# Kernel optimization log

Measured on AMD Instinct MI355X. Metric: run time of the kernel, lower is better.

The kernel has to match this reference:

```python
import jax, jax.numpy as jnp
import numpy as np

N1, N2 = 262144, 65536          # dense / coarse point counts (packed batch)
PREV, SKIP, M0, M1 = 512, 256, 256, 256
EPS_BN = 1e-5                    # torch BatchNorm1d default eps
EPS_DIST = 1e-8


def _bn(x, g, b):
    # BatchNorm1d in training mode: biased batch stats over the point axis
    m = x.mean(axis=0)
    v = x.var(axis=0)
    return (x - m) * jax.lax.rsqrt(v + EPS_BN) * g + b


def setup_inputs() -> dict:
    key = jax.random.key(0)
    ks = jax.random.split(key, 8)
    inp = {
        "points1": jax.random.normal(ks[0], (N1, SKIP), jnp.float32),
        "points2": jax.random.normal(ks[1], (N2, PREV), jnp.float32),
        "dist": jax.random.uniform(ks[2], (N1, 3), jnp.float32),
        "idx": jax.random.randint(ks[3], (N1, 3), 0, N2, dtype=jnp.int32),
        # mlp_f0 / norm_f0
        "Wf0": jax.random.normal(ks[4], (PREV, M0), jnp.float32) / np.sqrt(PREV).astype(np.float32),
        "bf0": jnp.zeros((M0,), jnp.float32),
        "gf0": jnp.ones((M0,), jnp.float32),
        "betaf0": jnp.zeros((M0,), jnp.float32),
        # mlp_s0 / norm_s0 (skip path)
        "Ws0": jax.random.normal(ks[5], (SKIP, M0), jnp.float32) / np.sqrt(SKIP).astype(np.float32),
        "bs0": jnp.zeros((M0,), jnp.float32),
        "gs0": jnp.ones((M0,), jnp.float32),
        "betas0": jnp.zeros((M0,), jnp.float32),
        # mlp_convs[0] / mlp_bns[0]
        "W1": jax.random.normal(ks[6], (M0, M1), jnp.float32) / np.sqrt(M0).astype(np.float32),
        "b1": jnp.zeros((M1,), jnp.float32),
        "g1": jnp.ones((M1,), jnp.float32),
        "beta1": jnp.zeros((M1,), jnp.float32),
    }
    return inp


def reference(points1, points2, dist, idx, Wf0, bf0, gf0, betaf0,
              Ws0, bs0, gs0, betas0, W1, b1, g1, beta1):
    # f0 MLP + BN on coarse features: [N2, PREV] -> [N2, M0]
    p2 = _bn(points2 @ Wf0 + bf0, gf0, betaf0)
    # inverse-distance weights over 3 neighbors: [N1, 3]
    dr = 1.0 / (dist + EPS_DIST)
    w = dr / dr.sum(axis=1, keepdims=True)
    # fused gather + weighted sum: p2[idx] is [N1, 3, M0]
    interp = jnp.einsum('nkc,nk->nc', p2[idx], w)
    # skip path: [N1, SKIP] -> [N1, M0]
    skip = _bn(points1 @ Ws0 + bs0, gs0, betas0)
    x = jax.nn.relu(interp + skip)
    # mlp_convs stack (one layer here): Linear + BN + ReLU
    x = jax.nn.relu(_bn(x @ W1 + b1, g1, beta1))
    return x
```

## Files before the change

kernel.cpp:

```cpp
#include <hip/hip_runtime.h>
#include <hip/hip_bf16.h>

#define CN1 262144
#define CN2 65536
#define CPREV 512
#define CSKIP 256

using u16 = unsigned short;

typedef __attribute__((ext_vector_type(8))) short short8;
typedef __attribute__((ext_vector_type(8))) unsigned short ushort8;
typedef __attribute__((ext_vector_type(4))) float f32x4;
typedef __attribute__((ext_vector_type(8))) float f32x8;

__device__ __forceinline__ float toF(float v) { return v; }
__device__ __forceinline__ float toF(u16 u) { return __uint_as_float(((unsigned)u) << 16); }
__device__ __forceinline__ u16 f2bf(float f) {
    unsigned b = __float_as_uint(f);
    b += 0x7FFFu + ((b >> 16) & 1u);
    return (u16)(b >> 16);
}
__device__ __forceinline__ unsigned pack2(float lo, float hi) {
    return ((unsigned)f2bf(hi) << 16) | (unsigned)f2bf(lo);
}

__global__ __launch_bounds__(256) void transpose_all(
    const float* __restrict__ Wf0, const float* __restrict__ Ws0,
    const float* __restrict__ W1,
    u16* __restrict__ Wtf0, u16* __restrict__ Wts0, u16* __restrict__ Wt1)
{
    int b = blockIdx.x;
    const float* W; u16* Wt; int ksh, e;
    if (b < 512)      { W = Wf0; Wt = Wtf0; ksh = 9; e = b * 256 + threadIdx.x; }
    else if (b < 768) { W = Ws0; Wt = Wts0; ksh = 8; e = (b - 512) * 256 + threadIdx.x; }
    else              { W = W1;  Wt = Wt1;  ksh = 8; e = (b - 768) * 256 + threadIdx.x; }
    int K = 1 << ksh;
    int n = e >> ksh;
    int k = e & (K - 1);
    Wt[e] = f2bf(W[((size_t)k << 8) + n]);
}

template<typename OT>
__device__ __forceinline__ void epilogue(
    f32x4 (&acc)[4][4], u16* AsU, u16* BsU,
    const float* __restrict__ bias, OT* __restrict__ C,
    float* __restrict__ partial, int bm, int t)
{
    const int lane = t & 63;
    const int wid = t >> 6;
    const int wrow = wid >> 2;
    const int wcol = wid & 3;
    __syncthreads();
    float* cs  = (float*)AsU;
    float* cs2 = ((float*)AsU) + 512;
    const int r4 = (lane >> 4) * 4;
    const int cc = lane & 15;
    float bv[4];
#pragma unroll
    for (int ni = 0; ni < 4; ++ni) bv[ni] = bias[wcol * 64 + ni * 16 + cc];

#pragma unroll
    for (int ni = 0; ni < 4; ++ni) {
        int col = wcol * 64 + ni * 16 + cc;
        float s = 0.f, s2 = 0.f;
#pragma unroll
        for (int mi = 0; mi < 4; ++mi) {
#pragma unroll
            for (int j = 0; j < 4; ++j) {
                float val = acc[mi][ni][j] + bv[ni];
                s += val;
                s2 = fmaf(val, val, s2);
            }
        }
        s  += __shfl_xor(s, 16);  s  += __shfl_xor(s, 32);
        s2 += __shfl_xor(s2, 16); s2 += __shfl_xor(s2, 32);
        if (lane < 16) { cs[wrow * 256 + col] = s; cs2[wrow * 256 + col] = s2; }
    }

    if constexpr (sizeof(OT) == 2) {
        u16* patchw = BsU + wid * (16 * 72);
        const int trow = lane >> 2;
        const int c16 = (lane & 3) * 16;
#pragma unroll
        for (int mi = 0; mi < 4; ++mi) {
            __syncthreads();
#pragma unroll
            for (int ni = 0; ni < 4; ++ni)
#pragma unroll
                for (int j = 0; j < 4; ++j)
                    patchw[(r4 + j) * 72 + ni * 16 + cc] = f2bf(acc[mi][ni][j] + bv[ni]);
            __syncthreads();
            ushort8 u0 = *(const ushort8*)&patchw[trow * 72 + c16];
            ushort8 u1 = *(const ushort8*)&patchw[trow * 72 + c16 + 8];
            size_t r = (size_t)bm + wrow * 64 + mi * 16 + trow;
            size_t cb = (size_t)wcol * 64 + c16;
            *(ushort8*)((u16*)C + r * 256 + cb) = u0;
            *(ushort8*)((u16*)C + r * 256 + cb + 8) = u1;
        }
    } else {
        float* patchf = ((float*)BsU) + wid * (16 * 36);
        const int trow = lane >> 2;
        const int c8 = (lane & 3) * 8;
#pragma unroll
        for (int mi = 0; mi < 4; ++mi) {
#pragma unroll
            for (int np = 0; np < 2; ++np) {
                __syncthreads();
#pragma unroll
                for (int h = 0; h < 2; ++h) {
                    int ni = np * 2 + h;
#pragma unroll
                    for (int j = 0; j < 4; ++j)
                        patchf[(r4 + j) * 36 + h * 16 + cc] = acc[mi][ni][j] + bv[ni];
                }
                __syncthreads();
                float4 v0 = *(float4*)&patchf[trow * 36 + c8];
                float4 v1 = *(float4*)&patchf[trow * 36 + c8 + 4];
                size_t r = (size_t)bm + wrow * 64 + mi * 16 + trow;
                size_t cb = (size_t)wcol * 64 + np * 32 + c8;
                *(float4*)((float*)C + r * 256 + cb) = v0;
                *(float4*)((float*)C + r * 256 + cb + 4) = v1;
            }
        }
    }
    __syncthreads();
    if (t < 256) {
        partial[(size_t)blockIdx.x * 512 + t]       = cs[t] + cs[256 + t];
        partial[(size_t)blockIdx.x * 512 + 256 + t] = cs2[t] + cs2[256 + t];
    }
}

template<int K, typename OT>
__global__ __launch_bounds__(512) void gemm_mfma(
    const float* __restrict__ Af, const u16* __restrict__ Wt,
    const float* __restrict__ bias, OT* __restrict__ C,
    float* __restrict__ partial)
{
    __shared__ u16 As0[128 * 40], As1[128 * 40];
    __shared__ u16 Bs0[256 * 40], Bs1[256 * 40];
    const int t = threadIdx.x;
    const int bm = blockIdx.x * 128;
    const int lane = t & 63;
    const int wid = t >> 6;
    const int wrow = wid >> 2;
    const int wcol = wid & 3;

    const int arow = t >> 2;
    const int koff = (t & 3) * 8;

    f32x4 acc[4][4] = {};

    float4 ga0A, ga1A, ga0B, ga1B;
    ushort8 gb0A, gb1A, gb0B, gb1B;

    auto LOADA = [&](int k0) {
        const float* p = Af + (size_t)(bm + arow) * K + k0 + koff;
        ga0A = *(const float4*)p;
        ga1A = *(const float4*)(p + 4);
        const u16* q = Wt + (size_t)arow * K + k0 + koff;
        gb0A = *(const ushort8*)q;
        gb1A = *(const ushort8*)(q + (size_t)128 * K);
    };
    auto LOADB = [&](int k0) {
        const float* p = Af + (size_t)(bm + arow) * K + k0 + koff;
        ga0B = *(const float4*)p;
        ga1B = *(const float4*)(p + 4);
        const u16* q = Wt + (size_t)arow * K + k0 + koff;
        gb0B = *(const ushort8*)q;
        gb1B = *(const ushort8*)(q + (size_t)128 * K);
    };
    auto STAGE = [&](u16* as, u16* bs, const float4& g0, const float4& g1,
                     const ushort8& b0, const ushort8& b1) {
        uint4 w;
        w.x = pack2(g0.x, g0.y);
        w.y = pack2(g0.z, g0.w);
        w.z = pack2(g1.x, g1.y);
        w.w = pack2(g1.z, g1.w);
        *(uint4*)&as[arow * 40 + koff] = w;
        *(ushort8*)&bs[arow * 40 + koff] = b0;
        *(ushort8*)&bs[(128 + arow) * 40 + koff] = b1;
    };
    auto MMA = [&](const u16* as, const u16* bs) {
        const int kq = (lane >> 4) * 8;
        const int rr = lane & 15;
        short8 af[4];
#pragma unroll
        for (int mi = 0; mi < 4; ++mi)
            af[mi] = *(const short8*)&as[(wrow * 64 + mi * 16 + rr) * 40 + kq];
#pragma unroll
        for (int ni = 0; ni < 4; ++ni) {
            short8 bf = *(const short8*)&bs[(wcol * 64 + ni * 16 + rr) * 40 + kq];
#pragma unroll
            for (int mi = 0; mi < 4; ++mi)
                acc[mi][ni] = __builtin_amdgcn_mfma_f32_16x16x32_bf16(
                    af[mi], bf, acc[mi][ni], 0, 0, 0);
        }
    };

    constexpr int nk = K >> 5;
    LOADA(0);
    LOADB(32);
    STAGE(As0, Bs0, ga0A, ga1A, gb0A, gb1A);
    __syncthreads();

#define GM_STEP(IT)                                                           \
    if ((IT) < nk) {                                                          \
        if ((IT) + 2 < nk) {                                                  \
            if (((IT)&1) == 0) LOADA(((IT)+2) << 5); else LOADB(((IT)+2) << 5);\
        }                                                                     \
        if ((IT) + 1 < nk) {                                                  \
            if (((IT)&1) == 0) STAGE(As1, Bs1, ga0B, ga1B, gb0B, gb1B);       \
            else               STAGE(As0, Bs0, ga0A, ga1A, gb0A, gb1A);       \
        }                                                                     \
        MMA((((IT)&1) == 0) ? As0 : As1, (((IT)&1) == 0) ? Bs0 : Bs1);        \
        __syncthreads();                                                      \
    }
    GM_STEP(0)  GM_STEP(1)  GM_STEP(2)  GM_STEP(3)
    GM_STEP(4)  GM_STEP(5)  GM_STEP(6)  GM_STEP(7)
    GM_STEP(8)  GM_STEP(9)  GM_STEP(10) GM_STEP(11)
    GM_STEP(12) GM_STEP(13) GM_STEP(14) GM_STEP(15)
#undef GM_STEP

    epilogue<OT>(acc, As0, Bs0, bias, C, partial, bm, t);
}

template<typename OT>
__global__ __launch_bounds__(512) void gemm_fused(
    const u16* __restrict__ skipb, const u16* __restrict__ y2,
    const float* __restrict__ dist, const int* __restrict__ idx,
    const float* __restrict__ ssf, const float* __restrict__ sss,
    const u16* __restrict__ Wt, const float* __restrict__ bias,
    OT* __restrict__ C, float* __restrict__ partial)
{
    constexpr int K = 256;
    __shared__ u16 As0[128 * 40], As1[128 * 40];
    __shared__ u16 Bs0[256 * 40], Bs1[256 * 40];
    __shared__ float sstab[768];
    const int t = threadIdx.x;
    const int bm = blockIdx.x * 128;
    const int lane = t & 63;
    const int wid = t >> 6;
    const int wrow = wid >> 2;
    const int wcol = wid & 3;

    const int arow = t >> 2;
    const int koff = (t & 3) * 8;
    const int row = bm + arow;

    for (int e = t; e < 768; e += 512)
        sstab[e] = (e < 256) ? ssf[e] : sss[e - 256];

    float d0 = dist[row * 3 + 0], d1 = dist[row * 3 + 1], d2 = dist[row * 3 + 2];
    float r0 = 1.f / (d0 + 1e-8f), r1 = 1.f / (d1 + 1e-8f), r2 = 1.f / (d2 + 1e-8f);
    float inv = 1.f / (r0 + r1 + r2);
    const float w0 = r0 * inv, w1 = r1 * inv, w2 = r2 * inv;
    const size_t i0 = (size_t)idx[row * 3 + 0];
    const size_t i1 = (size_t)idx[row * 3 + 1];
    const size_t i2 = (size_t)idx[row * 3 + 2];

    f32x4 acc[4][4] = {};

    ushort8 skA, a0A, a1A, a2A, gb0A, gb1A;
    ushort8 skB, a0B, a1B, a2B, gb0B, gb1B;

    auto LOADA = [&](int k0) {
        const int kc = k0 + koff;
        skA = *(const ushort8*)(skipb + (size_t)row * 256 + kc);
        a0A = *(const ushort8*)(y2 + i0 * 256 + kc);
        a1A = *(const ushort8*)(y2 + i1 * 256 + kc);
        a2A = *(const ushort8*)(y2 + i2 * 256 + kc);
        const u16* q = Wt + (size_t)arow * K + kc;
        gb0A = *(const ushort8*)q;
        gb1A = *(const ushort8*)(q + (size_t)128 * K);
    };
    auto LOADB = [&](int k0) {
        const int kc = k0 + koff;
        skB = *(const ushort8*)(skipb + (size_t)row * 256 + kc);
        a0B = *(const ushort8*)(y2 + i0 * 256 + kc);
        a1B = *(const ushort8*)(y2 + i1 * 256 + kc);
        a2B = *(const ushort8*)(y2 + i2 * 256 + kc);
        const u16* q = Wt + (size_t)arow * K + kc;
        gb0B = *(const ushort8*)q;
        gb1B = *(const ushort8*)(q + (size_t)128 * K);
    };
    auto STAGE = [&](u16* as, u16* bs, int kstep, const ushort8& sk8,
                     const ushort8& a0, const ushort8& a1, const ushort8& a2,
                     const ushort8& b0, const ushort8& b1) {
        const int kc = (kstep << 5) + koff;
        f32x8 sf = *(const f32x8*)&sstab[kc];
        f32x8 sx = *(const f32x8*)&sstab[256 + kc];
        f32x8 ch = *(const f32x8*)&sstab[512 + kc];
        float xs[8];
#pragma unroll
        for (int j = 0; j < 8; ++j) {
            float iv = w0 * toF((u16)a0[j]) + w1 * toF((u16)a1[j])
                     + w2 * toF((u16)a2[j]);
            float val = fmaf(iv, sf[j], fmaf(toF((u16)sk8[j]), sx[j], ch[j]));
            xs[j] = fmaxf(val, 0.f);
        }
        uint4 w;
        w.x = pack2(xs[0], xs[1]);
        w.y = pack2(xs[2], xs[3]);
        w.z = pack2(xs[4], xs[5]);
        w.w = pack2(xs[6], xs[7]);
        *(uint4*)&as[arow * 40 + koff] = w;
        *(ushort8*)&bs[arow * 40 + koff] = b0;
        *(ushort8*)&bs[(128 + arow) * 40 + koff] = b1;
    };
    auto MMA = [&](const u16* as, const u16* bs) {
        const int kq = (lane >> 4) * 8;
        const int rr = lane & 15;
        short8 af[4];
#pragma unroll
        for (int mi = 0; mi < 4; ++mi)
            af[mi] = *(const short8*)&as[(wrow * 64 + mi * 16 + rr) * 40 + kq];
#pragma unroll
        for (int ni = 0; ni < 4; ++ni) {
            short8 bf = *(const short8*)&bs[(wcol * 64 + ni * 16 + rr) * 40 + kq];
#pragma unroll
            for (int mi = 0; mi < 4; ++mi)
                acc[mi][ni] = __builtin_amdgcn_mfma_f32_16x16x32_bf16(
                    af[mi], bf, acc[mi][ni], 0, 0, 0);
        }
    };

    constexpr int nk = K >> 5;
    LOADA(0);
    LOADB(32);
    __syncthreads();
    STAGE(As0, Bs0, 0, skA, a0A, a1A, a2A, gb0A, gb1A);
    __syncthreads();

#define GF_STEP(IT)                                                           \
    if ((IT) < nk) {                                                          \
        if ((IT) + 2 < nk) {                                                  \
            if (((IT)&1) == 0) LOADA(((IT)+2) << 5); else LOADB(((IT)+2) << 5);\
        }                                                                     \
        if ((IT) + 1 < nk) {                                                  \
            if (((IT)&1) == 0)                                                \
                STAGE(As1, Bs1, (IT)+1, skB, a0B, a1B, a2B, gb0B, gb1B);      \
            else                                                              \
                STAGE(As0, Bs0, (IT)+1, skA, a0A, a1A, a2A, gb0A, gb1A);      \
        }                                                                     \
        MMA((((IT)&1) == 0) ? As0 : As1, (((IT)&1) == 0) ? Bs0 : Bs1);        \
        __syncthreads();                                                      \
    }
    GF_STEP(0) GF_STEP(1) GF_STEP(2) GF_STEP(3)
    GF_STEP(4) GF_STEP(5) GF_STEP(6) GF_STEP(7)
#undef GF_STEP

    epilogue<OT>(acc, As0, Bs0, bias, C, partial, bm, t);
}

__global__ __launch_bounds__(256) void colstats_final_par(
    const float* __restrict__ partial, int nb, float invR,
    const float* __restrict__ g, const float* __restrict__ beta,
    const float* __restrict__ fold, float* __restrict__ ss)
{
    int c = blockIdx.x;
    int t = threadIdx.x;
    float s = 0.f, s2 = 0.f;
    for (int b = t; b < nb; b += 256) {
        s  += partial[(size_t)b * 512 + c];
        s2 += partial[(size_t)b * 512 + 256 + c];
    }
#pragma unroll
    for (int o = 32; o > 0; o >>= 1) {
        s += __shfl_xor(s, o);
        s2 += __shfl_xor(s2, o);
    }
    __shared__ float rs[4], rs2[4];
    if ((t & 63) == 0) { rs[t >> 6] = s; rs2[t >> 6] = s2; }
    __syncthreads();
    if (t == 0) {
        float S  = rs[0] + rs[1] + rs[2] + rs[3];
        float S2 = rs2[0] + rs2[1] + rs2[2] + rs2[3];
        float m = S * invR;
        float var = fmaf(-m, m, S2 * invR);
        float scale = g[c] * rsqrtf(var + 1e-5f);
        float shift = fmaf(-m, scale, beta[c]);
        if (fold) shift += fold[256 + c];
        ss[c] = scale;
        ss[256 + c] = shift;
    }
}

__global__ __launch_bounds__(256) void bn_relu_cvt(
    const u16* __restrict__ y3, float* __restrict__ out,
    const float* __restrict__ ss)
{
    size_t e = ((size_t)blockIdx.x * 256 + threadIdx.x) * 8;
    int kc = (int)(e & 255);
    ushort8 v = *(const ushort8*)(y3 + e);
    f32x8 sc = *(const f32x8*)(ss + kc);
    f32x8 sh = *(const f32x8*)(ss + 256 + kc);
    float4 o0, o1;
    o0.x = fmaxf(fmaf(toF((u16)v[0]), sc[0], sh[0]), 0.f);
    o0.y = fmaxf(fmaf(toF((u16)v[1]), sc[1], sh[1]), 0.f);
    o0.z = fmaxf(fmaf(toF((u16)v[2]), sc[2], sh[2]), 0.f);
    o0.w = fmaxf(fmaf(toF((u16)v[3]), sc[3], sh[3]), 0.f);
    o1.x = fmaxf(fmaf(toF((u16)v[4]), sc[4], sh[4]), 0.f);
    o1.y = fmaxf(fmaf(toF((u16)v[5]), sc[5], sh[5]), 0.f);
    o1.z = fmaxf(fmaf(toF((u16)v[6]), sc[6], sh[6]), 0.f);
    o1.w = fmaxf(fmaf(toF((u16)v[7]), sc[7], sh[7]), 0.f);
    *(float4*)(out + e) = o0;
    *(float4*)(out + e + 4) = o1;
}

__global__ __launch_bounds__(256) void bn_relu_inplace(
    float* __restrict__ out, const float* __restrict__ ss)
{
    size_t i4 = (size_t)blockIdx.x * 256 + threadIdx.x;
    int c4 = (int)(i4 & 63);
    float4 v = reinterpret_cast<float4*>(out)[i4];
    float4 sc = reinterpret_cast<const float4*>(ss)[c4];
    float4 sh = reinterpret_cast<const float4*>(ss + 256)[c4];
    v.x = fmaxf(fmaf(v.x, sc.x, sh.x), 0.f);
    v.y = fmaxf(fmaf(v.y, sc.y, sh.y), 0.f);
    v.z = fmaxf(fmaf(v.z, sc.z, sh.z), 0.f);
    v.w = fmaxf(fmaf(v.w, sc.w, sh.w), 0.f);
    reinterpret_cast<float4*>(out)[i4] = v;
}

extern "C" void kernel_launch(void* const* d_in, const int* in_sizes, int n_in,
                              void* d_out, int out_size, void* d_ws, size_t ws_size,
                              hipStream_t stream) {
    const float* points1 = (const float*)d_in[0];
    const float* points2 = (const float*)d_in[1];
    const float* dist    = (const float*)d_in[2];
    const int*   idx     = (const int*)d_in[3];
    const float* Wf0     = (const float*)d_in[4];
    const float* bf0     = (const float*)d_in[5];
    const float* gf0     = (const float*)d_in[6];
    const float* betaf0  = (const float*)d_in[7];
    const float* Ws0     = (const float*)d_in[8];
    const float* bs0     = (const float*)d_in[9];
    const float* gs0     = (const float*)d_in[10];
    const float* betas0  = (const float*)d_in[11];
    const float* W1      = (const float*)d_in[12];
    const float* b1      = (const float*)d_in[13];
    const float* g1      = (const float*)d_in[14];
    const float* beta1   = (const float*)d_in[15];

    u16* ws = (u16*)d_ws;
    size_t off = 0;
    u16* y2   = ws + off;  off += (size_t)CN2 * 256;
    u16* xbuf = ws + off;  off += (size_t)CN1 * 256;
    u16* Wtf0 = ws + off;  off += 512 * 256;
    u16* Wts0 = ws + off;  off += 256 * 256;
    u16* Wt1  = ws + off;  off += 256 * 256;
    float* partial = (float*)(ws + off); off += (size_t)2048 * 512 * 2;
    float* ss_f0 = (float*)(ws + off); off += 1024;
    float* ss_s0 = (float*)(ws + off); off += 1024;
    float* ss_1  = (float*)(ws + off); off += 1024;
    u16* y3 = ws + off;
    const size_t NEED = (off + (size_t)CN1 * 256) * 2;
    const bool fused_y3 = (ws_size >= NEED);
    float* out = (float*)d_out;

    transpose_all<<<1024, 256, 0, stream>>>(Wf0, Ws0, W1, Wtf0, Wts0, Wt1);

    gemm_mfma<512, u16><<<CN2 / 128, 512, 0, stream>>>(
        points2, Wtf0, bf0, y2, partial);
    colstats_final_par<<<256, 256, 0, stream>>>(partial, CN2 / 128, 1.0f / CN2,
                                                gf0, betaf0, nullptr, ss_f0);
    gemm_mfma<256, u16><<<CN1 / 128, 512, 0, stream>>>(
        points1, Wts0, bs0, xbuf, partial);
    colstats_final_par<<<256, 256, 0, stream>>>(partial, CN1 / 128, 1.0f / CN1,
                                                gs0, betas0, ss_f0, ss_s0);
    if (fused_y3) {
        gemm_fused<u16><<<CN1 / 128, 512, 0, stream>>>(
            xbuf, y2, dist, idx, ss_f0, ss_s0, Wt1, b1, y3, partial);
    } else {
        gemm_fused<float><<<CN1 / 128, 512, 0, stream>>>(
            xbuf, y2, dist, idx, ss_f0, ss_s0, Wt1, b1, out, partial);
    }
    colstats_final_par<<<256, 256, 0, stream>>>(partial, CN1 / 128, 1.0f / CN1,
                                                g1, beta1, nullptr, ss_1);
    if (fused_y3) {
        bn_relu_cvt<<<32768, 256, 0, stream>>>(y3, out, ss_1);
    } else {
        bn_relu_inplace<<<CN1 / 4, 256, 0, stream>>>(out, ss_1);
    }
}
```

Baseline: 416.7 us.

## Load GEMM weight fragments directly from global into registers, drop B LDS staging

Both MFMA GEMM kernels no longer stage weight tiles through shared memory. Each wave now loads its bf16 B fragments straight from global memory into double-buffered registers, one k-step ahead. The epilogue reuses the A buffers for its patch scratch, and the BN partial-sum write moves ahead of the output stores. The kernels also get minimum-occupancy launch bounds. This cuts LDS traffic and footprint and removes B-tile LDS stores, but adds redundant global/L2 weight reads per wave. The occupancy bounds may force register spills given the 64-register accumulator.

```diff
diff --git a/kernel.cpp b/kernel.cpp
--- a/kernel.cpp
+++ b/kernel.cpp
@@ -42,7 +42,7 @@
 
 template<typename OT>
 __device__ __forceinline__ void epilogue(
-    f32x4 (&acc)[4][4], u16* AsU, u16* BsU,
+    f32x4 (&acc)[4][4], u16* As0, u16* As1,
     const float* __restrict__ bias, OT* __restrict__ C,
     float* __restrict__ partial, int bm, int t)
 {
@@ -51,8 +51,8 @@
     const int wrow = wid >> 2;
     const int wcol = wid & 3;
     __syncthreads();
-    float* cs  = (float*)AsU;
-    float* cs2 = ((float*)AsU) + 512;
+    float* cs  = (float*)As0;
+    float* cs2 = ((float*)As0) + 512;
     const int r4 = (lane >> 4) * 4;
     const int cc = lane & 15;
     float bv[4];
@@ -76,9 +76,14 @@
         s2 += __shfl_xor(s2, 16); s2 += __shfl_xor(s2, 32);
         if (lane < 16) { cs[wrow * 256 + col] = s; cs2[wrow * 256 + col] = s2; }
     }
+    __syncthreads();
+    if (t < 256) {
+        partial[(size_t)blockIdx.x * 512 + t]       = cs[t] + cs[256 + t];
+        partial[(size_t)blockIdx.x * 512 + 256 + t] = cs2[t] + cs2[256 + t];
+    }
 
     if constexpr (sizeof(OT) == 2) {
-        u16* patchw = BsU + wid * (16 * 72);
+        u16* patchw = (wid < 4) ? (As0 + wid * 1152) : (As1 + (wid - 4) * 1152);
         const int trow = lane >> 2;
         const int c16 = (lane & 3) * 16;
 #pragma unroll
@@ -98,7 +103,7 @@
             *(ushort8*)((u16*)C + r * 256 + cb + 8) = u1;
         }
     } else {
-        float* patchf = ((float*)BsU) + wid * (16 * 36);
+        float* patchf = (float*)((wid < 4) ? (As0 + wid * 1152) : (As1 + (wid - 4) * 1152));
         const int trow = lane >> 2;
         const int c8 = (lane & 3) * 8;
 #pragma unroll
@@ -123,21 +128,15 @@
             }
         }
     }
-    __syncthreads();
-    if (t < 256) {
-        partial[(size_t)blockIdx.x * 512 + t]       = cs[t] + cs[256 + t];
-        partial[(size_t)blockIdx.x * 512 + 256 + t] = cs2[t] + cs2[256 + t];
-    }
 }
 
 template<int K, typename OT>
-__global__ __launch_bounds__(512) void gemm_mfma(
+__global__ __launch_bounds__(512, 4) void gemm_mfma(
     const float* __restrict__ Af, const u16* __restrict__ Wt,
     const float* __restrict__ bias, OT* __restrict__ C,
     float* __restrict__ partial)
 {
     __shared__ u16 As0[128 * 40], As1[128 * 40];
-    __shared__ u16 Bs0[256 * 40], Bs1[256 * 40];
     const int t = threadIdx.x;
     const int bm = blockIdx.x * 128;
     const int lane = t & 63;
@@ -147,73 +146,69 @@
 
     const int arow = t >> 2;
     const int koff = (t & 3) * 8;
+    const int rr = lane & 15;
+    const int kq = (lane >> 4) * 8;
+    const u16* Wb = Wt + (size_t)(wcol * 64 + rr) * K + kq;
 
     f32x4 acc[4][4] = {};
 
     float4 ga0A, ga1A, ga0B, ga1B;
-    ushort8 gb0A, gb1A, gb0B, gb1B;
+    short8 bfA[4], bfB[4];
 
     auto LOADA = [&](int k0) {
         const float* p = Af + (size_t)(bm + arow) * K + k0 + koff;
         ga0A = *(const float4*)p;
         ga1A = *(const float4*)(p + 4);
-        const u16* q = Wt + (size_t)arow * K + k0 + koff;
-        gb0A = *(const ushort8*)q;
-        gb1A = *(const ushort8*)(q + (size_t)128 * K);
     };
     auto LOADB = [&](int k0) {
         const float* p = Af + (size_t)(bm + arow) * K + k0 + koff;
         ga0B = *(const float4*)p;
         ga1B = *(const float4*)(p + 4);
-        const u16* q = Wt + (size_t)arow * K + k0 + koff;
-        gb0B = *(const ushort8*)q;
-        gb1B = *(const ushort8*)(q + (size_t)128 * K);
-    };
-    auto STAGE = [&](u16* as, u16* bs, const float4& g0, const float4& g1,
-                     const ushort8& b0, const ushort8& b1) {
+    };
+    auto LOADBF = [&](int k0, short8 (&bf)[4]) {
+#pragma unroll
+        for (int ni = 0; ni < 4; ++ni)
+            bf[ni] = *(const short8*)(Wb + (size_t)ni * 16 * K + k0);
+    };
+    auto STAGE = [&](u16* as, const float4& g0, const float4& g1) {
         uint4 w;
         w.x = pack2(g0.x, g0.y);
         w.y = pack2(g0.z, g0.w);
         w.z = pack2(g1.x, g1.y);
         w.w = pack2(g1.z, g1.w);
         *(uint4*)&as[arow * 40 + koff] = w;
-        *(ushort8*)&bs[arow * 40 + koff] = b0;
-        *(ushort8*)&bs[(128 + arow) * 40 + koff] = b1;
-    };
-    auto MMA = [&](const u16* as, const u16* bs) {
-        const int kq = (lane >> 4) * 8;
-        const int rr = lane & 15;
+    };
+    auto MMA = [&](const u16* as, const short8 (&bf)[4]) {
         short8 af[4];
 #pragma unroll
         for (int mi = 0; mi < 4; ++mi)
             af[mi] = *(const short8*)&as[(wrow * 64 + mi * 16 + rr) * 40 + kq];
 #pragma unroll
-        for (int ni = 0; ni < 4; ++ni) {
-            short8 bf = *(const short8*)&bs[(wcol * 64 + ni * 16 + rr) * 40 + kq];
+        for (int ni = 0; ni < 4; ++ni)
 #pragma unroll
             for (int mi = 0; mi < 4; ++mi)
                 acc[mi][ni] = __builtin_amdgcn_mfma_f32_16x16x32_bf16(
-                    af[mi], bf, acc[mi][ni], 0, 0, 0);
-        }
+                    af[mi], bf[ni], acc[mi][ni], 0, 0, 0);
     };
 
     constexpr int nk = K >> 5;
     LOADA(0);
     LOADB(32);
-    STAGE(As0, Bs0, ga0A, ga1A, gb0A, gb1A);
-    __syncthreads();
-
-#define GM_STEP(IT)                                                           \
-    if ((IT) < nk) {                                                          \
-        if ((IT) + 2 < nk) {                                                  \
-            if (((IT)&1) == 0) LOADA(((IT)+2) << 5); else LOADB(((IT)+2) << 5);\
-        }                                                                     \
-        if ((IT) + 1 < nk) {                                                  \
-            if (((IT)&1) == 0) STAGE(As1, Bs1, ga0B, ga1B, gb0B, gb1B);       \
-            else               STAGE(As0, Bs0, ga0A, ga1A, gb0A, gb1A);       \
-        }                                                                     \
-        MMA((((IT)&1) == 0) ? As0 : As1, (((IT)&1) == 0) ? Bs0 : Bs1);        \
-        __syncthreads();                                                      \
+    STAGE(As0, ga0A, ga1A);
+    LOADBF(0, bfA);
+    __syncthreads();
+
+#define GM_STEP(IT)                                                             \
+    if ((IT) < nk) {                                                            \
+        if ((IT) + 2 < nk) {                                                    \
+            if (((IT)&1) == 0) LOADA(((IT)+2) << 5); else LOADB(((IT)+2) << 5); \
+        }                                                                       \
+        if ((IT) + 1 < nk) {                                                    \
+            if (((IT)&1) == 0) { STAGE(As1, ga0B, ga1B); LOADBF(((IT)+1) << 5, bfB); } \
+            else               { STAGE(As0, ga0A, ga1A); LOADBF(((IT)+1) << 5, bfA); } \
+        }                                                                       \
+        if (((IT)&1) == 0) MMA(As0, bfA); else MMA(As1, bfB);                   \
+        __syncthreads();                                                        \
     }
     GM_STEP(0)  GM_STEP(1)  GM_STEP(2)  GM_STEP(3)
     GM_STEP(4)  GM_STEP(5)  GM_STEP(6)  GM_STEP(7)
@@ -221,11 +216,11 @@
     GM_STEP(12) GM_STEP(13) GM_STEP(14) GM_STEP(15)
 #undef GM_STEP
 
-    epilogue<OT>(acc, As0, Bs0, bias, C, partial, bm, t);
+    epilogue<OT>(acc, As0, As1, bias, C, partial, bm, t);
 }
 
 template<typename OT>
-__global__ __launch_bounds__(512) void gemm_fused(
+__global__ __launch_bounds__(512, 3) void gemm_fused(
     const u16* __restrict__ skipb, const u16* __restrict__ y2,
     const float* __restrict__ dist, const int* __restrict__ idx,
     const float* __restrict__ ssf, const float* __restrict__ sss,
@@ -234,7 +229,6 @@
 {
     constexpr int K = 256;
     __shared__ u16 As0[128 * 40], As1[128 * 40];
-    __shared__ u16 Bs0[256 * 40], Bs1[256 * 40];
     __shared__ float sstab[768];
     const int t = threadIdx.x;
     const int bm = blockIdx.x * 128;
@@ -246,6 +240,9 @@
     const int arow = t >> 2;
     const int koff = (t & 3) * 8;
     const int row = bm + arow;
+    const int rr = lane & 15;
+    const int kq = (lane >> 4) * 8;
+    const u16* Wb = Wt + (size_t)(wcol * 64 + rr) * K + kq;
 
     for (int e = t; e < 768; e += 512)
         sstab[e] = (e < 256) ? ssf[e] : sss[e - 256];
@@ -254,38 +251,37 @@
     float r0 = 1.f / (d0 + 1e-8f), r1 = 1.f / (d1 + 1e-8f), r2 = 1.f / (d2 + 1e-8f);
     float inv = 1.f / (r0 + r1 + r2);
     const float w0 = r0 * inv, w1 = r1 * inv, w2 = r2 * inv;
-    const size_t i0 = (size_t)idx[row * 3 + 0];
-    const size_t i1 = (size_t)idx[row * 3 + 1];
-    const size_t i2 = (size_t)idx[row * 3 + 2];
+    const unsigned i0 = (unsigned)idx[row * 3 + 0];
+    const unsigned i1 = (unsigned)idx[row * 3 + 1];
+    const unsigned i2 = (unsigned)idx[row * 3 + 2];
 
     f32x4 acc[4][4] = {};
 
-    ushort8 skA, a0A, a1A, a2A, gb0A, gb1A;
-    ushort8 skB, a0B, a1B, a2B, gb0B, gb1B;
+    ushort8 skA, a0A, a1A, a2A;
+    ushort8 skB, a0B, a1B, a2B;
+    short8 bfA[4], bfB[4];
 
     auto LOADA = [&](int k0) {
         const int kc = k0 + koff;
         skA = *(const ushort8*)(skipb + (size_t)row * 256 + kc);
-        a0A = *(const ushort8*)(y2 + i0 * 256 + kc);
-        a1A = *(const ushort8*)(y2 + i1 * 256 + kc);
-        a2A = *(const ushort8*)(y2 + i2 * 256 + kc);
-        const u16* q = Wt + (size_t)arow * K + kc;
-        gb0A = *(const ushort8*)q;
-        gb1A = *(const ushort8*)(q + (size_t)128 * K);
+        a0A = *(const ushort8*)(y2 + (size_t)i0 * 256 + kc);
+        a1A = *(const ushort8*)(y2 + (size_t)i1 * 256 + kc);
+        a2A = *(const ushort8*)(y2 + (size_t)i2 * 256 + kc);
     };
     auto LOADB = [&](int k0) {
         const int kc = k0 + koff;
         skB = *(const ushort8*)(skipb + (size_t)row * 256 + kc);
-        a0B = *(const ushort8*)(y2 + i0 * 256 + kc);
-        a1B = *(const ushort8*)(y2 + i1 * 256 + kc);
-        a2B = *(const ushort8*)(y2 + i2 * 256 + kc);
-        const u16* q = Wt + (size_t)arow * K + kc;
-        gb0B = *(const ushort8*)q;
-        gb1B = *(const ushort8*)(q + (size_t)128 * K);
-    };
-    auto STAGE = [&](u16* as, u16* bs, int kstep, const ushort8& sk8,
-                     const ushort8& a0, const ushort8& a1, const ushort8& a2,
-                     const ushort8& b0, const ushort8& b1) {
+        a0B = *(const ushort8*)(y2 + (size_t)i0 * 256 + kc);
+        a1B = *(const ushort8*)(y2 + (size_t)i1 * 256 + kc);
+        a2B = *(const ushort8*)(y2 + (size_t)i2 * 256 + kc);
+    };
+    auto LOADBF = [&](int k0, short8 (&bf)[4]) {
+#pragma unroll
+        for (int ni = 0; ni < 4; ++ni)
+            bf[ni] = *(const short8*)(Wb + (size_t)ni * 16 * K + k0);
+    };
+    auto STAGE = [&](u16* as, int kstep, const ushort8& sk8,
+                     const ushort8& a0, const ushort8& a1, const ushort8& a2) {
         const int kc = (kstep << 5) + koff;
         f32x8 sf = *(const f32x8*)&sstab[kc];
         f32x8 sx = *(const f32x8*)&sstab[256 + kc];
@@ -304,52 +300,47 @@
         w.z = pack2(xs[4], xs[5]);
         w.w = pack2(xs[6], xs[7]);
         *(uint4*)&as[arow * 40 + koff] = w;
-        *(ushort8*)&bs[arow * 40 + koff] = b0;
-        *(ushort8*)&bs[(128 + arow) * 40 + koff] = b1;
-    };
-    auto MMA = [&](const u16* as, const u16* bs) {
-        const int kq = (lane >> 4) * 8;
-        const int rr = lane & 15;
+    };
+    auto MMA = [&](const u16* as, const short8 (&bf)[4]) {
         short8 af[4];
 #pragma unroll
         for (int mi = 0; mi < 4; ++mi)
             af[mi] = *(const short8*)&as[(wrow * 64 + mi * 16 + rr) * 40 + kq];
 #pragma unroll
-        for (int ni = 0; ni < 4; ++ni) {
-            short8 bf = *(const short8*)&bs[(wcol * 64 + ni * 16 + rr) * 40 + kq];
+        for (int ni = 0; ni < 4; ++ni)
 #pragma unroll
             for (int mi = 0; mi < 4; ++mi)
                 acc[mi][ni] = __builtin_amdgcn_mfma_f32_16x16x32_bf16(
-                    af[mi], bf, acc[mi][ni], 0, 0, 0);
-        }
+                    af[mi], bf[ni], acc[mi][ni], 0, 0, 0);
     };
 
     constexpr int nk = K >> 5;
     LOADA(0);
     LOADB(32);
     __syncthreads();
-    STAGE(As0, Bs0, 0, skA, a0A, a1A, a2A, gb0A, gb1A);
-    __syncthreads();
-
-#define GF_STEP(IT)                                                           \
-    if ((IT) < nk) {                                                          \
-        if ((IT) + 2 < nk) {                                                  \
-            if (((IT)&1) == 0) LOADA(((IT)+2) << 5); else LOADB(((IT)+2) << 5);\
-        }                                                                     \
-        if ((IT) + 1 < nk) {                                                  \
-            if (((IT)&1) == 0)                                                \
-                STAGE(As1, Bs1, (IT)+1, skB, a0B, a1B, a2B, gb0B, gb1B);      \
-            else                                                              \
-                STAGE(As0, Bs0, (IT)+1, skA, a0A, a1A, a2A, gb0A, gb1A);      \
-        }                                                                     \
-        MMA((((IT)&1) == 0) ? As0 : As1, (((IT)&1) == 0) ? Bs0 : Bs1);        \
-        __syncthreads();                                                      \
+    STAGE(As0, 0, skA, a0A, a1A, a2A);
+    LOADBF(0, bfA);
+    __syncthreads();
+
+#define GF_STEP(IT)                                                             \
+    if ((IT) < nk) {                                                            \
+        if ((IT) + 2 < nk) {                                                    \
+            if (((IT)&1) == 0) LOADA(((IT)+2) << 5); else LOADB(((IT)+2) << 5); \
+        }                                                                       \
+        if ((IT) + 1 < nk) {                                                    \
+            if (((IT)&1) == 0) { STAGE(As1, (IT)+1, skB, a0B, a1B, a2B);        \
+                                 LOADBF(((IT)+1) << 5, bfB); }                  \
+            else               { STAGE(As0, (IT)+1, skA, a0A, a1A, a2A);        \
+                                 LOADBF(((IT)+1) << 5, bfA); }                  \
+        }                                                                       \
+        if (((IT)&1) == 0) MMA(As0, bfA); else MMA(As1, bfB);                   \
+        __syncthreads();                                                        \
     }
     GF_STEP(0) GF_STEP(1) GF_STEP(2) GF_STEP(3)
     GF_STEP(4) GF_STEP(5) GF_STEP(6) GF_STEP(7)
 #undef GF_STEP
 
-    epilogue<OT>(acc, As0, Bs0, bias, C, partial, bm, t);
+    epilogue<OT>(acc, As0, As1, bias, C, partial, bm, t);
 }
 
 __global__ __launch_bounds__(256) void colstats_final_par(
```

Result: slower. 479.3 us (+15.0%).

## Double GEMM block size to 16 waves with split A/B loader roles

Applied to the files above, without the earlier changes.

The three MFMA GEMM kernels now launch 1024 threads per block instead of 512, with each wave computing a 32x64 tile rather than 64x64, which halves the accumulator registers per thread. The first 512 threads load and convert the A operand while the other 512 load the weight tile, so the per-thread global-load and staging work is split. The epilogue is adapted to 16 waves, writing column-stat partials earlier and using both B buffers as transpose patches. This is meant to give more waves to hide memory latency, at the cost of larger block-wide barriers and halving the fragment reuse per wave.

```diff
diff --git a/kernel.cpp b/kernel.cpp
--- a/kernel.cpp
+++ b/kernel.cpp
@@ -41,8 +41,8 @@
 }
 
 template<typename OT>
-__device__ __forceinline__ void epilogue(
-    f32x4 (&acc)[4][4], u16* AsU, u16* BsU,
+__device__ __forceinline__ void epilogue16(
+    f32x4 (&acc)[2][4], u16* As0, u16* Bs0, u16* Bs1,
     const float* __restrict__ bias, OT* __restrict__ C,
     float* __restrict__ partial, int bm, int t)
 {
@@ -51,8 +51,8 @@
     const int wrow = wid >> 2;
     const int wcol = wid & 3;
     __syncthreads();
-    float* cs  = (float*)AsU;
-    float* cs2 = ((float*)AsU) + 512;
+    float* cs  = (float*)As0;
+    float* cs2 = cs + 1024;
     const int r4 = (lane >> 4) * 4;
     const int cc = lane & 15;
     float bv[4];
@@ -64,7 +64,7 @@
         int col = wcol * 64 + ni * 16 + cc;
         float s = 0.f, s2 = 0.f;
 #pragma unroll
-        for (int mi = 0; mi < 4; ++mi) {
+        for (int mi = 0; mi < 2; ++mi) {
 #pragma unroll
             for (int j = 0; j < 4; ++j) {
                 float val = acc[mi][ni][j] + bv[ni];
@@ -76,13 +76,20 @@
         s2 += __shfl_xor(s2, 16); s2 += __shfl_xor(s2, 32);
         if (lane < 16) { cs[wrow * 256 + col] = s; cs2[wrow * 256 + col] = s2; }
     }
+    __syncthreads();
+    if (t < 256) {
+        partial[(size_t)blockIdx.x * 512 + t] =
+            cs[t] + cs[256 + t] + cs[512 + t] + cs[768 + t];
+        partial[(size_t)blockIdx.x * 512 + 256 + t] =
+            cs2[t] + cs2[256 + t] + cs2[512 + t] + cs2[768 + t];
+    }
 
     if constexpr (sizeof(OT) == 2) {
-        u16* patchw = BsU + wid * (16 * 72);
+        u16* patchw = (wid < 8) ? (Bs0 + wid * 1152) : (Bs1 + (wid - 8) * 1152);
         const int trow = lane >> 2;
         const int c16 = (lane & 3) * 16;
 #pragma unroll
-        for (int mi = 0; mi < 4; ++mi) {
+        for (int mi = 0; mi < 2; ++mi) {
             __syncthreads();
 #pragma unroll
             for (int ni = 0; ni < 4; ++ni)
@@ -92,17 +99,17 @@
             __syncthreads();
             ushort8 u0 = *(const ushort8*)&patchw[trow * 72 + c16];
             ushort8 u1 = *(const ushort8*)&patchw[trow * 72 + c16 + 8];
-            size_t r = (size_t)bm + wrow * 64 + mi * 16 + trow;
+            size_t r = (size_t)bm + wrow * 32 + mi * 16 + trow;
             size_t cb = (size_t)wcol * 64 + c16;
             *(ushort8*)((u16*)C + r * 256 + cb) = u0;
             *(ushort8*)((u16*)C + r * 256 + cb + 8) = u1;
         }
     } else {
-        float* patchf = ((float*)BsU) + wid * (16 * 36);
+        float* patchf = (float*)((wid < 8) ? (Bs0 + wid * 1152) : (Bs1 + (wid - 8) * 1152));
         const int trow = lane >> 2;
         const int c8 = (lane & 3) * 8;
 #pragma unroll
-        for (int mi = 0; mi < 4; ++mi) {
+        for (int mi = 0; mi < 2; ++mi) {
 #pragma unroll
             for (int np = 0; np < 2; ++np) {
                 __syncthreads();
@@ -116,22 +123,17 @@
                 __syncthreads();
                 float4 v0 = *(float4*)&patchf[trow * 36 + c8];
                 float4 v1 = *(float4*)&patchf[trow * 36 + c8 + 4];
-                size_t r = (size_t)bm + wrow * 64 + mi * 16 + trow;
+                size_t r = (size_t)bm + wrow * 32 + mi * 16 + trow;
                 size_t cb = (size_t)wcol * 64 + np * 32 + c8;
                 *(float4*)((float*)C + r * 256 + cb) = v0;
                 *(float4*)((float*)C + r * 256 + cb + 4) = v1;
             }
         }
     }
-    __syncthreads();
-    if (t < 256) {
-        partial[(size_t)blockIdx.x * 512 + t]       = cs[t] + cs[256 + t];
-        partial[(size_t)blockIdx.x * 512 + 256 + t] = cs2[t] + cs2[256 + t];
-    }
 }
 
 template<int K, typename OT>
-__global__ __launch_bounds__(512) void gemm_mfma(
+__global__ __launch_bounds__(1024, 4) void gemm_mfma(
     const float* __restrict__ Af, const u16* __restrict__ Wt,
     const float* __restrict__ bias, OT* __restrict__ C,
     float* __restrict__ partial)
@@ -144,54 +146,67 @@
     const int wid = t >> 6;
     const int wrow = wid >> 2;
     const int wcol = wid & 3;
+    const bool stA = t < 512;
 
     const int arow = t >> 2;
     const int koff = (t & 3) * 8;
-
-    f32x4 acc[4][4] = {};
+    const int u = t - 512;
+    const int brow = u >> 1;
+    const int bk = (u & 1) * 16;
+    const int rr = lane & 15;
+    const int kq = (lane >> 4) * 8;
+
+    f32x4 acc[2][4] = {};
 
     float4 ga0A, ga1A, ga0B, ga1B;
     ushort8 gb0A, gb1A, gb0B, gb1B;
 
     auto LOADA = [&](int k0) {
-        const float* p = Af + (size_t)(bm + arow) * K + k0 + koff;
-        ga0A = *(const float4*)p;
-        ga1A = *(const float4*)(p + 4);
-        const u16* q = Wt + (size_t)arow * K + k0 + koff;
-        gb0A = *(const ushort8*)q;
-        gb1A = *(const ushort8*)(q + (size_t)128 * K);
+        if (stA) {
+            const float* p = Af + (size_t)(bm + arow) * K + k0 + koff;
+            ga0A = *(const float4*)p;
+            ga1A = *(const float4*)(p + 4);
+        } else {
+            const u16* q = Wt + (size_t)brow * K + k0 + bk;
+            gb0A = *(const ushort8*)q;
+            gb1A = *(const ushort8*)(q + 8);
+        }
     };
     auto LOADB = [&](int k0) {
-        const float* p = Af + (size_t)(bm + arow) * K + k0 + koff;
-        ga0B = *(const float4*)p;
-        ga1B = *(const float4*)(p + 4);
-        const u16* q = Wt + (size_t)arow * K + k0 + koff;
-        gb0B = *(const ushort8*)q;
-        gb1B = *(const ushort8*)(q + (size_t)128 * K);
+        if (stA) {
+            const float* p = Af + (size_t)(bm + arow) * K + k0 + koff;
+            ga0B = *(const float4*)p;
+            ga1B = *(const float4*)(p + 4);
+        } else {
+            const u16* q = Wt + (size_t)brow * K + k0 + bk;
+            gb0B = *(const ushort8*)q;
+            gb1B = *(const ushort8*)(q + 8);
+        }
     };
     auto STAGE = [&](u16* as, u16* bs, const float4& g0, const float4& g1,
                      const ushort8& b0, const ushort8& b1) {
-        uint4 w;
-        w.x = pack2(g0.x, g0.y);
-        w.y = pack2(g0.z, g0.w);
-        w.z = pack2(g1.x, g1.y);
-        w.w = pack2(g1.z, g1.w);
-        *(uint4*)&as[arow * 40 + koff] = w;
-        *(ushort8*)&bs[arow * 40 + koff] = b0;
-        *(ushort8*)&bs[(128 + arow) * 40 + koff] = b1;
+        if (stA) {
+            uint4 w;
+            w.x = pack2(g0.x, g0.y);
+            w.y = pack2(g0.z, g0.w);
+            w.z = pack2(g1.x, g1.y);
+            w.w = pack2(g1.z, g1.w);
+            *(uint4*)&as[arow * 40 + koff] = w;
+        } else {
+            *(ushort8*)&bs[brow * 40 + bk] = b0;
+            *(ushort8*)&bs[brow * 40 + bk + 8] = b1;
+        }
     };
     auto MMA = [&](const u16* as, const u16* bs) {
-        const int kq = (lane >> 4) * 8;
-        const int rr = lane & 15;
-        short8 af[4];
-#pragma unroll
-        for (int mi = 0; mi < 4; ++mi)
-            af[mi] = *(const short8*)&as[(wrow * 64 + mi * 16 + rr) * 40 + kq];
+        short8 af[2];
+#pragma unroll
+        for (int mi = 0; mi < 2; ++mi)
+            af[mi] = *(const short8*)&as[(wrow * 32 + mi * 16 + rr) * 40 + kq];
 #pragma unroll
         for (int ni = 0; ni < 4; ++ni) {
             short8 bf = *(const short8*)&bs[(wcol * 64 + ni * 16 + rr) * 40 + kq];
 #pragma unroll
-            for (int mi = 0; mi < 4; ++mi)
+            for (int mi = 0; mi < 2; ++mi)
                 acc[mi][ni] = __builtin_amdgcn_mfma_f32_16x16x32_bf16(
                     af[mi], bf, acc[mi][ni], 0, 0, 0);
         }
@@ -203,17 +218,17 @@
     STAGE(As0, Bs0, ga0A, ga1A, gb0A, gb1A);
     __syncthreads();
 
-#define GM_STEP(IT)                                                           \
-    if ((IT) < nk) {                                                          \
-        if ((IT) + 2 < nk) {                                                  \
-            if (((IT)&1) == 0) LOADA(((IT)+2) << 5); else LOADB(((IT)+2) << 5);\
-        }                                                                     \
-        if ((IT) + 1 < nk) {                                                  \
-            if (((IT)&1) == 0) STAGE(As1, Bs1, ga0B, ga1B, gb0B, gb1B);       \
-            else               STAGE(As0, Bs0, ga0A, ga1A, gb0A, gb1A);       \
-        }                                                                     \
-        MMA((((IT)&1) == 0) ? As0 : As1, (((IT)&1) == 0) ? Bs0 : Bs1);        \
-        __syncthreads();                                                      \
+#define GM_STEP(IT)                                                              \
+    if ((IT) < nk) {                                                             \
+        if ((IT) + 2 < nk) {                                                     \
+            if (((IT)&1) == 0) LOADA(((IT)+2) << 5); else LOADB(((IT)+2) << 5);  \
+        }                                                                        \
+        if ((IT) + 1 < nk) {                                                     \
+            if (((IT)&1) == 0) STAGE(As1, Bs1, ga0B, ga1B, gb0B, gb1B);          \
+            else               STAGE(As0, Bs0, ga0A, ga1A, gb0A, gb1A);          \
+        }                                                                        \
+        if (((IT)&1) == 0) MMA(As0, Bs0); else MMA(As1, Bs1);                    \
+        __syncthreads();                                                         \
     }
     GM_STEP(0)  GM_STEP(1)  GM_STEP(2)  GM_STEP(3)
     GM_STEP(4)  GM_STEP(5)  GM_STEP(6)  GM_STEP(7)
@@ -221,11 +236,11 @@
     GM_STEP(12) GM_STEP(13) GM_STEP(14) GM_STEP(15)
 #undef GM_STEP
 
-    epilogue<OT>(acc, As0, Bs0, bias, C, partial, bm, t);
+    epilogue16<OT>(acc, As0, Bs0, Bs1, bias, C, partial, bm, t);
 }
 
 template<typename OT>
-__global__ __launch_bounds__(512) void gemm_fused(
+__global__ __launch_bounds__(1024, 4) void gemm_fused(
     const u16* __restrict__ skipb, const u16* __restrict__ y2,
     const float* __restrict__ dist, const int* __restrict__ idx,
     const float* __restrict__ ssf, const float* __restrict__ sss,
@@ -242,83 +257,101 @@
     const int wid = t >> 6;
     const int wrow = wid >> 2;
     const int wcol = wid & 3;
+    const bool stA = t < 512;
 
     const int arow = t >> 2;
     const int koff = (t & 3) * 8;
-    const int row = bm + arow;
-
-    for (int e = t; e < 768; e += 512)
-        sstab[e] = (e < 256) ? ssf[e] : sss[e - 256];
-
-    float d0 = dist[row * 3 + 0], d1 = dist[row * 3 + 1], d2 = dist[row * 3 + 2];
-    float r0 = 1.f / (d0 + 1e-8f), r1 = 1.f / (d1 + 1e-8f), r2 = 1.f / (d2 + 1e-8f);
-    float inv = 1.f / (r0 + r1 + r2);
-    const float w0 = r0 * inv, w1 = r1 * inv, w2 = r2 * inv;
-    const size_t i0 = (size_t)idx[row * 3 + 0];
-    const size_t i1 = (size_t)idx[row * 3 + 1];
-    const size_t i2 = (size_t)idx[row * 3 + 2];
-
-    f32x4 acc[4][4] = {};
-
-    ushort8 skA, a0A, a1A, a2A, gb0A, gb1A;
-    ushort8 skB, a0B, a1B, a2B, gb0B, gb1B;
+    const int u = t - 512;
+    const int brow = u >> 1;
+    const int bk = (u & 1) * 16;
+    const int rr = lane & 15;
+    const int kq = (lane >> 4) * 8;
+
+    if (t < 768) sstab[t] = (t < 256) ? ssf[t] : sss[t - 256];
+
+    float w0 = 0.f, w1 = 0.f, w2 = 0.f;
+    unsigned i0 = 0, i1 = 0, i2 = 0;
+    int row = 0;
+    if (stA) {
+        row = bm + arow;
+        float d0 = dist[row * 3 + 0], d1 = dist[row * 3 + 1], d2 = dist[row * 3 + 2];
+        float r0 = 1.f / (d0 + 1e-8f), r1 = 1.f / (d1 + 1e-8f), r2 = 1.f / (d2 + 1e-8f);
+        float inv = 1.f / (r0 + r1 + r2);
+        w0 = r0 * inv; w1 = r1 * inv; w2 = r2 * inv;
+        i0 = (unsigned)idx[row * 3 + 0];
+        i1 = (unsigned)idx[row * 3 + 1];
+        i2 = (unsigned)idx[row * 3 + 2];
+    }
+
+    f32x4 acc[2][4] = {};
+
+    ushort8 skA, a0A, a1A, a2A;
+    ushort8 skB, a0B, a1B, a2B;
+    ushort8 gb0A, gb1A, gb0B, gb1B;
 
     auto LOADA = [&](int k0) {
-        const int kc = k0 + koff;
-        skA = *(const ushort8*)(skipb + (size_t)row * 256 + kc);
-        a0A = *(const ushort8*)(y2 + i0 * 256 + kc);
-        a1A = *(const ushort8*)(y2 + i1 * 256 + kc);
-        a2A = *(const ushort8*)(y2 + i2 * 256 + kc);
-        const u16* q = Wt + (size_t)arow * K + kc;
-        gb0A = *(const ushort8*)q;
-        gb1A = *(const ushort8*)(q + (size_t)128 * K);
+        if (stA) {
+            const int kc = k0 + koff;
+            skA = *(const ushort8*)(skipb + (size_t)row * 256 + kc);
+            a0A = *(const ushort8*)(y2 + (size_t)i0 * 256 + kc);
+            a1A = *(const ushort8*)(y2 + (size_t)i1 * 256 + kc);
+            a2A = *(const ushort8*)(y2 + (size_t)i2 * 256 + kc);
+        } else {
+            const u16* q = Wt + (size_t)brow * K + k0 + bk;
+            gb0A = *(const ushort8*)q;
+            gb1A = *(const ushort8*)(q + 8);
+        }
     };
     auto LOADB = [&](int k0) {
-        const int kc = k0 + koff;
-        skB = *(const ushort8*)(skipb + (size_t)row * 256 + kc);
-        a0B = *(const ushort8*)(y2 + i0 * 256 + kc);
-        a1B = *(const ushort8*)(y2 + i1 * 256 + kc);
-        a2B = *(const ushort8*)(y2 + i2 * 256 + kc);
-        const u16* q = Wt + (size_t)arow * K + kc;
-        gb0B = *(const ushort8*)q;
-        gb1B = *(const ushort8*)(q + (size_t)128 * K);
+        if (stA) {
+            const int kc = k0 + koff;
+            skB = *(const ushort8*)(skipb + (size_t)row * 256 + kc);
+            a0B = *(const ushort8*)(y2 + (size_t)i0 * 256 + kc);
+            a1B = *(const ushort8*)(y2 + (size_t)i1 * 256 + kc);
+            a2B = *(const ushort8*)(y2 + (size_t)i2 * 256 + kc);
+        } else {
+            const u16* q = Wt + (size_t)brow * K + k0 + bk;
+            gb0B = *(const ushort8*)q;
+            gb1B = *(const ushort8*)(q + 8);
+        }
     };
     auto STAGE = [&](u16* as, u16* bs, int kstep, const ushort8& sk8,
                      const ushort8& a0, const ushort8& a1, const ushort8& a2,
                      const ushort8& b0, const ushort8& b1) {
-        const int kc = (kstep << 5) + koff;
-        f32x8 sf = *(const f32x8*)&sstab[kc];
-        f32x8 sx = *(const f32x8*)&sstab[256 + kc];
-        f32x8 ch = *(const f32x8*)&sstab[512 + kc];
-        float xs[8];
-#pragma unroll
-        for (int j = 0; j < 8; ++j) {
-            float iv = w0 * toF((u16)a0[j]) + w1 * toF((u16)a1[j])
-                     + w2 * toF((u16)a2[j]);
-            float val = fmaf(iv, sf[j], fmaf(toF((u16)sk8[j]), sx[j], ch[j]));
-            xs[j] = fmaxf(val, 0.f);
-        }
-        uint4 w;
-        w.x = pack2(xs[0], xs[1]);
-        w.y = pack2(xs[2], xs[3]);
-        w.z = pack2(xs[4], xs[5]);
-        w.w = pack2(xs[6], xs[7]);
-        *(uint4*)&as[arow * 40 + koff] = w;
-        *(ushort8*)&bs[arow * 40 + koff] = b0;
-        *(ushort8*)&bs[(128 + arow) * 40 + koff] = b1;
+        if (stA) {
+            const int kc = (kstep << 5) + koff;
+            f32x8 sf = *(const f32x8*)&sstab[kc];
+            f32x8 sx = *(const f32x8*)&sstab[256 + kc];
+            f32x8 ch = *(const f32x8*)&sstab[512 + kc];
+            float xs[8];
+#pragma unroll
+            for (int j = 0; j < 8; ++j) {
+                float iv = w0 * toF((u16)a0[j]) + w1 * toF((u16)a1[j])
+                         + w2 * toF((u16)a2[j]);
+                float val = fmaf(iv, sf[j], fmaf(toF((u16)sk8[j]), sx[j], ch[j]));
+                xs[j] = fmaxf(val, 0.f);
+            }
+            uint4 w;
+            w.x = pack2(xs[0], xs[1]);
+            w.y = pack2(xs[2], xs[3]);
+            w.z = pack2(xs[4], xs[5]);
+            w.w = pack2(xs[6], xs[7]);
+            *(uint4*)&as[arow * 40 + koff] = w;
+        } else {
+            *(ushort8*)&bs[brow * 40 + bk] = b0;
+            *(ushort8*)&bs[brow * 40 + bk + 8] = b1;
+        }
     };
     auto MMA = [&](const u16* as, const u16* bs) {
-        const int kq = (lane >> 4) * 8;
-        const int rr = lane & 15;
-        short8 af[4];
-#pragma unroll
-        for (int mi = 0; mi < 4; ++mi)
-            af[mi] = *(const short8*)&as[(wrow * 64 + mi * 16 + rr) * 40 + kq];
+        short8 af[2];
+#pragma unroll
+        for (int mi = 0; mi < 2; ++mi)
+            af[mi] = *(const short8*)&as[(wrow * 32 + mi * 16 + rr) * 40 + kq];
 #pragma unroll
         for (int ni = 0; ni < 4; ++ni) {
             short8 bf = *(const short8*)&bs[(wcol * 64 + ni * 16 + rr) * 40 + kq];
 #pragma unroll
-            for (int mi = 0; mi < 4; ++mi)
+            for (int mi = 0; mi < 2; ++mi)
                 acc[mi][ni] = __builtin_amdgcn_mfma_f32_16x16x32_bf16(
                     af[mi], bf, acc[mi][ni], 0, 0, 0);
         }
@@ -331,25 +364,25 @@
     STAGE(As0, Bs0, 0, skA, a0A, a1A, a2A, gb0A, gb1A);
     __syncthreads();
 
-#define GF_STEP(IT)                                                           \
-    if ((IT) < nk) {                                                          \
-        if ((IT) + 2 < nk) {                                                  \
-            if (((IT)&1) == 0) LOADA(((IT)+2) << 5); else LOADB(((IT)+2) << 5);\
-        }                                                                     \
-        if ((IT) + 1 < nk) {                                                  \
-            if (((IT)&1) == 0)                                                \
-                STAGE(As1, Bs1, (IT)+1, skB, a0B, a1B, a2B, gb0B, gb1B);      \
-            else                                                              \
-                STAGE(As0, Bs0, (IT)+1, skA, a0A, a1A, a2A, gb0A, gb1A);      \
-        }                                                                     \
-        MMA((((IT)&1) == 0) ? As0 : As1, (((IT)&1) == 0) ? Bs0 : Bs1);        \
-        __syncthreads();                                                      \
+#define GF_STEP(IT)                                                              \
+    if ((IT) < nk) {                                                             \
+        if ((IT) + 2 < nk) {                                                     \
+            if (((IT)&1) == 0) LOADA(((IT)+2) << 5); else LOADB(((IT)+2) << 5);  \
+        }                                                                        \
+        if ((IT) + 1 < nk) {                                                     \
+            if (((IT)&1) == 0)                                                   \
+                STAGE(As1, Bs1, (IT)+1, skB, a0B, a1B, a2B, gb0B, gb1B);         \
+            else                                                                 \
+                STAGE(As0, Bs0, (IT)+1, skA, a0A, a1A, a2A, gb0A, gb1A);         \
+        }                                                                        \
+        if (((IT)&1) == 0) MMA(As0, Bs0); else MMA(As1, Bs1);                    \
+        __syncthreads();                                                         \
     }
     GF_STEP(0) GF_STEP(1) GF_STEP(2) GF_STEP(3)
     GF_STEP(4) GF_STEP(5) GF_STEP(6) GF_STEP(7)
 #undef GF_STEP
 
-    epilogue<OT>(acc, As0, Bs0, bias, C, partial, bm, t);
+    epilogue16<OT>(acc, As0, Bs0, Bs1, bias, C, partial, bm, t);
 }
 
 __global__ __launch_bounds__(256) void colstats_final_par(
@@ -460,19 +493,19 @@
 
     transpose_all<<<1024, 256, 0, stream>>>(Wf0, Ws0, W1, Wtf0, Wts0, Wt1);
 
-    gemm_mfma<512, u16><<<CN2 / 128, 512, 0, stream>>>(
+    gemm_mfma<512, u16><<<CN2 / 128, 1024, 0, stream>>>(
         points2, Wtf0, bf0, y2, partial);
     colstats_final_par<<<256, 256, 0, stream>>>(partial, CN2 / 128, 1.0f / CN2,
                                                 gf0, betaf0, nullptr, ss_f0);
-    gemm_mfma<256, u16><<<CN1 / 128, 512, 0, stream>>>(
+    gemm_mfma<256, u16><<<CN1 / 128, 1024, 0, stream>>>(
         points1, Wts0, bs0, xbuf, partial);
     colstats_final_par<<<256, 256, 0, stream>>>(partial, CN1 / 128, 1.0f / CN1,
                                                 gs0, betas0, ss_f0, ss_s0);
     if (fused_y3) {
-        gemm_fused<u16><<<CN1 / 128, 512, 0, stream>>>(
+        gemm_fused<u16><<<CN1 / 128, 1024, 0, stream>>>(
             xbuf, y2, dist, idx, ss_f0, ss_s0, Wt1, b1, y3, partial);
     } else {
-        gemm_fused<float><<<CN1 / 128, 512, 0, stream>>>(
+        gemm_fused<float><<<CN1 / 128, 1024, 0, stream>>>(
             xbuf, y2, dist, idx, ss_f0, ss_s0, Wt1, b1, out, partial);
     }
     colstats_final_par<<<256, 256, 0, stream>>>(partial, CN1 / 128, 1.0f / CN1,
```

Result: slower. 544.9 us (+30.8%).
